# Kernel tuning notes

Measured on AMD Instinct MI355X. Metric: run time of the kernel, lower is better.

Reference implementation:

```python
import jax, jax.numpy as jnp
import numpy as np

K1 = 3                      # spline kernel size per pseudo dim
SIZE = float(np.sqrt(2.0))  # pseudo_cartesian normalization size


def spline_weights(p, k):
    """Degree-1 open B-spline basis over 2D pseudo coords.
    p: [..., 2] in [0,1]. Returns basis [..., 4], weight_index [..., 4]."""
    v = jnp.clip(p, 0.0, 1.0) * (k - 1)
    lo = jnp.floor(v)
    frac = v - lo
    lo = lo.astype(jnp.int32)
    off = jnp.array([0, 1], dtype=jnp.int32)
    w0 = jnp.stack([1.0 - frac[..., 0], frac[..., 0]], axis=-1)   # [...,2]
    w1 = jnp.stack([1.0 - frac[..., 1], frac[..., 1]], axis=-1)   # [...,2]
    i0 = jnp.clip(lo[..., 0:1] + off, 0, k - 1)                    # [...,2]
    i1 = jnp.clip(lo[..., 1:2] + off, 0, k - 1)                    # [...,2]
    basis = (w0[..., :, None] * w1[..., None, :]).reshape(*p.shape[:-1], 4)
    widx = (i0[..., :, None] + k * i1[..., None, :]).reshape(*p.shape[:-1], 4)
    return basis, widx


def setup_inputs() -> dict:
    key = jax.random.key(0)
    kx, ke, kp, kq, kw, kb = jax.random.split(key, 6)
    N, C, P, E, K = 50000, 64, 16, 800000, K1 * K1
    x = jax.random.normal(kx, (N, C), dtype=jnp.float32)
    pos = jax.random.uniform(kp, (N, 2), dtype=jnp.float32)
    pose = jax.random.normal(kq, (N, P, 2), dtype=jnp.float32)
    pose = pose / (jnp.linalg.norm(pose, axis=-1, keepdims=True) + 1e-8)  # unit pose vectors
    W = jax.random.normal(kw, (P, K, C), dtype=jnp.float32) / np.sqrt(C * 4.0)
    bias = jax.random.normal(kb, (P,), dtype=jnp.float32) * 0.01
    edge_index = jax.random.randint(ke, (2, E), 0, N, dtype=jnp.int64)
    return {"x": x, "pos": pos, "pose": pose, "W": W, "bias": bias,
            "edge_index": edge_index}


def reference(x, pos, pose, W, bias, edge_index):
    N, C = x.shape
    P = pose.shape[1]
    row, col = edge_index[0], edge_index[1]
    # pseudo_cartesian: normalized relative position in [0,1]^2
    pseudo = (pos[col] - pos[row]) / (2.0 * SIZE) + 0.5              # [E,2]
    # posevec_to_rotmat on detached pose vectors
    pose_c = jax.lax.stop_gradient(pose)
    a, b = pose_c[..., 0], pose_c[..., 1]
    R = jnp.stack([jnp.stack([a, -b], -1), jnp.stack([b, a], -1)], -2)  # [N,P,2,2]
    Re = R[row]                                                      # [E,P,2,2]
    # rotate pseudo coords about (0.5, 0.5), batched over all poses
    p = jnp.einsum('epij,ej->epi', Re, pseudo - 0.5) + 0.5           # [E,P,2]
    basis, widx = spline_weights(p, K1)                              # [E,P,4]
    # SplineConv (out_channels=1, no root weight, no norm):
    # precompute per-node per-pose per-kernel-bin projections
    Z = jnp.einsum('nc,pkc->npk', x, W)                              # [N,P,K]
    pidx = jnp.arange(P)[None, :, None]
    vals = Z[col[:, None, None], pidx, widx]                         # [E,P,4]
    msg = jnp.sum(basis * vals, axis=-1)                             # [E,P]
    out = jax.ops.segment_sum(msg, row, num_segments=N)              # [N,P]
    return out + bias[None, :]
```

## Files before the change

### kernel.cpp

```cpp
#include <hip/hip_runtime.h>
#include <hip/hip_bf16.h>

#define C_DIM 64
#define P_DIM 16
#define K_DIM 9
#define INV2S 0.35355339059327373f

#define ZP_ROW 96
#define ZP_STRIDE 100
#define SH_FLOATS 6400

__device__ __forceinline__ unsigned bf_bits(float x) {
    unsigned u = __float_as_uint(x);
    return (u + 0x7fffu + ((u >> 16) & 1u)) >> 16;
}
__device__ __forceinline__ float bf_lo(unsigned w) { return __uint_as_float(w << 16); }
__device__ __forceinline__ float bf_hi(unsigned w) { return __uint_as_float(w & 0xffff0000u); }

__global__ __launch_bounds__(256) void z_gemm_kernel(const float* __restrict__ x,
                                                     const float* __restrict__ W,
                                                     const float* __restrict__ bias,
                                                     const float* __restrict__ pose,
                                                     float* __restrict__ out,
                                                     unsigned* __restrict__ Zp,
                                                     unsigned* __restrict__ poseb,
                                                     int N) {
    __shared__ float sh_raw[SH_FLOATS];
    float (*xs)[C_DIM + 4] = (float(*)[C_DIM + 4])sh_raw;
    unsigned* zs = (unsigned*)sh_raw;

    const int block_row = blockIdx.x * 64;
    const int tid = threadIdx.x;

    {
        const float4 b4 = ((const float4*)bias)[tid & 3];
        const int o4 = block_row * 4 + tid;
        if (o4 < N * 4) ((float4*)out)[o4] = b4;
    }

    #pragma unroll
    for (int j = 0; j < 4; ++j) {
        int idx = j * 256 + tid;
        int gr = block_row + (idx >> 4);
        int pp = idx & 15;
        if (gr < N) {
            float2 ab = ((const float2*)pose)[(size_t)gr * P_DIM + pp];
            poseb[(size_t)gr * P_DIM + pp] = bf_bits(ab.x) | (bf_bits(ab.y) << 16);
        }
    }

    for (int i = tid; i < C_DIM * (C_DIM / 4); i += 256) {
        int r = i >> 4, c4 = i & 15;
        int gr = block_row + r;
        float4 v = make_float4(0.0f, 0.0f, 0.0f, 0.0f);
        if (gr < N) v = ((const float4*)x)[(size_t)gr * (C_DIM / 4) + c4];
        *(float4*)&xs[r][c4 * 4] = v;
    }
    __syncthreads();

    const int rg = tid & 15;
    const int p  = tid >> 4;
    const int j0 = p * K_DIM;

    float acc[4][K_DIM];
    #pragma unroll
    for (int i = 0; i < 4; ++i)
        #pragma unroll
        for (int k = 0; k < K_DIM; ++k) acc[i][k] = 0.0f;

    const float4* W4 = (const float4*)W;
    #pragma unroll 4
    for (int cs = 0; cs < 16; ++cs) {
        float4 xv[4];
        #pragma unroll
        for (int i = 0; i < 4; ++i) xv[i] = *(const float4*)&xs[rg + 16 * i][cs * 4];
        #pragma unroll
        for (int k = 0; k < K_DIM; ++k) {
            float4 wv = W4[(size_t)(j0 + k) * (C_DIM / 4) + cs];
            #pragma unroll
            for (int i = 0; i < 4; ++i) {
                acc[i][k] = fmaf(xv[i].x, wv.x, acc[i][k]);
                acc[i][k] = fmaf(xv[i].y, wv.y, acc[i][k]);
                acc[i][k] = fmaf(xv[i].z, wv.z, acc[i][k]);
                acc[i][k] = fmaf(xv[i].w, wv.w, acc[i][k]);
            }
        }
    }
    __syncthreads();

    #pragma unroll
    for (int i = 0; i < 4; ++i) {
        unsigned* zrow = &zs[(rg + 16 * i) * ZP_STRIDE + p];
        #pragma unroll
        for (int i1 = 0; i1 < 3; ++i1)
            #pragma unroll
            for (int b0 = 0; b0 < 2; ++b0)
                zrow[(i1 * 2 + b0) * 16] =
                    bf_bits(acc[i][b0 + 3 * i1]) | (bf_bits(acc[i][b0 + 1 + 3 * i1]) << 16);
    }
    __syncthreads();

    const int nrow = min(64, N - block_row);
    float4* Zp4 = (float4*)Zp;
    const float4* zs4 = (const float4*)sh_raw;
    for (int i = tid; i < nrow * 24; i += 256) {
        int row = i / 24, q = i - row * 24;
        Zp4[(size_t)(block_row + row) * 24 + q] = zs4[row * (ZP_STRIDE / 4) + q];
    }
}

#define EILP 4
__global__ __launch_bounds__(256) void edge_kernel(const int* __restrict__ ei,
                                                   const float* __restrict__ pos,
                                                   const unsigned* __restrict__ poseb,
                                                   const unsigned* __restrict__ Zp,
                                                   float* __restrict__ out,
                                                   int E) {
    const int p  = threadIdx.x & 15;
    const int eg = threadIdx.x >> 4;
    const int e0 = blockIdx.x * (16 * EILP) + eg;

    int  r[EILP], c[EILP];
    bool valid[EILP];
    #pragma unroll
    for (int it = 0; it < EILP; ++it) {
        int e = e0 + it * 16;
        valid[it] = (e < E);
        int ec = valid[it] ? e : 0;
        r[it] = ei[ec];
        c[it] = ei[E + ec];
    }

    float d0[EILP], d1[EILP];
    #pragma unroll
    for (int it = 0; it < EILP; ++it) {
        const float2 pc = ((const float2*)pos)[c[it]];
        const float2 pr = ((const float2*)pos)[r[it]];
        d0[it] = (pc.x - pr.x) * INV2S;
        d1[it] = (pc.y - pr.y) * INV2S;
    }

    unsigned pw[EILP];
    #pragma unroll
    for (int it = 0; it < EILP; ++it)
        pw[it] = poseb[(size_t)r[it] * P_DIM + p];

    unsigned pa[EILP], pb[EILP];
    float f0[EILP], f1[EILP];
    #pragma unroll
    for (int it = 0; it < EILP; ++it) {
        const float a = bf_lo(pw[it]);
        const float b = bf_hi(pw[it]);
        const float p0 = fmaf(a, d0[it], fmaf(-b, d1[it], 0.5f));
        const float p1 = fmaf(b, d0[it], fmaf( a, d1[it], 0.5f));

        const float v0 = fminf(fmaxf(p0, 0.0f) * 2.0f, 1.9999999f);
        const float v1 = fminf(fmaxf(p1, 0.0f) * 2.0f, 1.9999999f);
        const float lo0 = floorf(v0);
        const float lo1 = floorf(v1);
        f0[it] = v0 - lo0;
        f1[it] = v1 - lo1;
        const int b0 = (int)lo0;
        const int b1 = (int)lo1;

        const unsigned* Zr = Zp + (size_t)c[it] * ZP_ROW + b1 * 32 + b0 * 16 + p;
        pa[it] = Zr[0];
        pb[it] = Zr[32];
    }

    #pragma unroll
    for (int it = 0; it < EILP; ++it) {
        const float za = bf_lo(pa[it]), zb = bf_hi(pa[it]);
        const float zc = bf_lo(pb[it]), zd = bf_hi(pb[it]);
        const float mlo = fmaf(f0[it], zb - za, za);
        const float mhi = fmaf(f0[it], zd - zc, zc);
        const float m   = fmaf(f1[it], mhi - mlo, mlo);
        if (valid[it]) atomicAdd(&out[(size_t)r[it] * P_DIM + p], m);
    }
}

extern "C" void kernel_launch(void* const* d_in, const int* in_sizes, int n_in,
                              void* d_out, int out_size, void* d_ws, size_t ws_size,
                              hipStream_t stream) {
    const float* x    = (const float*)d_in[0];
    const float* pos  = (const float*)d_in[1];
    const float* pose = (const float*)d_in[2];
    const float* W    = (const float*)d_in[3];
    const float* bias = (const float*)d_in[4];
    const int*   ei   = (const int*)d_in[5];

    const int N = in_sizes[0] / C_DIM;
    const int E = in_sizes[5] / 2;

    float* out = (float*)d_out;

    const size_t zp_bytes = (size_t)N * ZP_ROW * sizeof(unsigned);
    unsigned* Zp    = (unsigned*)d_ws;
    unsigned* poseb = (unsigned*)((char*)d_ws + zp_bytes);

    z_gemm_kernel<<<(N + 63) / 64, 256, 0, stream>>>(x, W, bias, pose, out, Zp, poseb, N);
    edge_kernel<<<(E + 16 * EILP - 1) / (16 * EILP), 256, 0, stream>>>(ei, pos, poseb, Zp, out, E);
}
```

Before: 164.9 us.

## Partition edge work by source-node slice to localize Zp gathers per block

The edge kernel now launches 2048 blocks as 256 edge chunks times 8 column slices. Each block scans its edge chunk and handles only edges whose source node falls in its slice, so the Zp rows it gathers come from a smaller node range and may stay cache-resident (possibly matched to the XCD layout). The cost is that every edge's column index is read 8 times. Instruction-level parallelism drops from 4 edges per thread to 1, and lanes whose edges fall outside the slice sit idle, causing heavy divergence.

```diff
diff --git a/kernel.cpp b/kernel.cpp
--- a/kernel.cpp
+++ b/kernel.cpp
@@ -9,6 +9,8 @@
 #define ZP_ROW 96
 #define ZP_STRIDE 100
 #define SH_FLOATS 6400
+
+#define EDGE_GROUPS 256
 
 __device__ __forceinline__ unsigned bf_bits(float x) {
     unsigned u = __float_as_uint(x);
@@ -109,73 +111,62 @@
     }
 }
 
-#define EILP 4
 __global__ __launch_bounds__(256) void edge_kernel(const int* __restrict__ ei,
                                                    const float* __restrict__ pos,
                                                    const unsigned* __restrict__ poseb,
                                                    const unsigned* __restrict__ Zp,
                                                    float* __restrict__ out,
-                                                   int E) {
+                                                   int E, int N) {
     const int p  = threadIdx.x & 15;
     const int eg = threadIdx.x >> 4;
-    const int e0 = blockIdx.x * (16 * EILP) + eg;
+    const int s     = blockIdx.x & 7;
+    const int group = blockIdx.x >> 3;
 
-    int  r[EILP], c[EILP];
-    bool valid[EILP];
-    #pragma unroll
-    for (int it = 0; it < EILP; ++it) {
-        int e = e0 + it * 16;
-        valid[it] = (e < E);
-        int ec = valid[it] ? e : 0;
-        r[it] = ei[ec];
-        c[it] = ei[E + ec];
-    }
+    const int chunk = (E + EDGE_GROUPS - 1) / EDGE_GROUPS;
+    const int eBeg = group * chunk;
+    const int eEnd = min(eBeg + chunk, E);
+    const int ns   = N >> 3;
+    const int cLo  = s * ns;
+    const int cHi  = (s == 7) ? N : cLo + ns;
 
-    float d0[EILP], d1[EILP];
-    #pragma unroll
-    for (int it = 0; it < EILP; ++it) {
-        const float2 pc = ((const float2*)pos)[c[it]];
-        const float2 pr = ((const float2*)pos)[r[it]];
-        d0[it] = (pc.x - pr.x) * INV2S;
-        d1[it] = (pc.y - pr.y) * INV2S;
-    }
+    for (int base = eBeg; base < eEnd; base += 16) {
+        const int e = base + eg;
+        const bool inrange = (e < eEnd);
+        const int c = inrange ? ei[E + e] : -1;
+        if (c < cLo || c >= cHi) continue;
 
-    unsigned pw[EILP];
-    #pragma unroll
-    for (int it = 0; it < EILP; ++it)
-        pw[it] = poseb[(size_t)r[it] * P_DIM + p];
+        const int r = ei[e];
+        const float2 pc = ((const float2*)pos)[c];
+        const float2 pr = ((const float2*)pos)[r];
+        const float d0 = (pc.x - pr.x) * INV2S;
+        const float d1 = (pc.y - pr.y) * INV2S;
 
-    unsigned pa[EILP], pb[EILP];
-    float f0[EILP], f1[EILP];
-    #pragma unroll
-    for (int it = 0; it < EILP; ++it) {
-        const float a = bf_lo(pw[it]);
-        const float b = bf_hi(pw[it]);
-        const float p0 = fmaf(a, d0[it], fmaf(-b, d1[it], 0.5f));
-        const float p1 = fmaf(b, d0[it], fmaf( a, d1[it], 0.5f));
+        const unsigned pw = poseb[(size_t)r * P_DIM + p];
+        const float a = bf_lo(pw);
+        const float b = bf_hi(pw);
+        const float p0 = fmaf(a, d0, fmaf(-b, d1, 0.5f));
+        const float p1 = fmaf(b, d0, fmaf( a, d1, 0.5f));
 
         const float v0 = fminf(fmaxf(p0, 0.0f) * 2.0f, 1.9999999f);
         const float v1 = fminf(fmaxf(p1, 0.0f) * 2.0f, 1.9999999f);
         const float lo0 = floorf(v0);
         const float lo1 = floorf(v1);
-        f0[it] = v0 - lo0;
-        f1[it] = v1 - lo1;
+        const float f0 = v0 - lo0;
+        const float f1 = v1 - lo1;
         const int b0 = (int)lo0;
         const int b1 = (int)lo1;
 
-        const unsigned* Zr = Zp + (size_t)c[it] * ZP_ROW + b1 * 32 + b0 * 16 + p;
-        pa[it] = Zr[0];
-        pb[it] = Zr[32];
-    }
+        const unsigned* Zr = Zp + (size_t)c * ZP_ROW + b1 * 32 + b0 * 16 + p;
+        const unsigned pa = Zr[0];
+        const unsigned pb = Zr[32];
 
-    #pragma unroll
-    for (int it = 0; it < EILP; ++it) {
-        const float za = bf_lo(pa[it]), zb = bf_hi(pa[it]);
-        const float zc = bf_lo(pb[it]), zd = bf_hi(pb[it]);
-        const float mlo = fmaf(f0[it], zb - za, za);
-        const float mhi = fmaf(f0[it], zd - zc, zc);
-        const float m   = fmaf(f1[it], mhi - mlo, mlo);
-        if (valid[it]) atomicAdd(&out[(size_t)r[it] * P_DIM + p], m);
+        const float za = bf_lo(pa), zb = bf_hi(pa);
+        const float zc = bf_lo(pb), zd = bf_hi(pb);
+        const float mlo = fmaf(f0, zb - za, za);
+        const float mhi = fmaf(f0, zd - zc, zc);
+        const float m   = fmaf(f1, mhi - mlo, mlo);
+
+        atomicAdd(&out[(size_t)r * P_DIM + p], m);
     }
 }
 
@@ -199,5 +190,5 @@
     unsigned* poseb = (unsigned*)((char*)d_ws + zp_bytes);
 
     z_gemm_kernel<<<(N + 63) / 64, 256, 0, stream>>>(x, W, bias, pose, out, Zp, poseb, N);
-    edge_kernel<<<(E + 16 * EILP - 1) / (16 * EILP), 256, 0, stream>>>(ei, pos, poseb, Zp, out, E);
+    edge_kernel<<<EDGE_GROUPS * 8, 256, 0, stream>>>(ei, pos, poseb, Zp, out, E, N);
 }
```

New measurement: 289.4 us. 75.5% more time.
